# Kernel tuning notes

Hardware: AMD Instinct MI355X
Metric: run time of the kernel (lower is better)

## Reference

```python
import jax, jax.numpy as jnp
import numpy as np

jax.config.update("jax_enable_x64", True)  # torch uses int64 labels with wrapping arithmetic

N = 100_000   # nodes
E = 3_200_000 # edges
D = 128       # label classes (argmax dim)
NUM_ITERATIONS = 3


def setup_inputs() -> dict:
    key = jax.random.key(0)
    k1, k2 = jax.random.split(key)
    x = jax.random.normal(k1, (N, D), dtype=jnp.float32)
    edge_index = jax.random.randint(k2, (2, E), 0, N, dtype=jnp.int64)
    return {"x": x, "edge_index": edge_index}


def _edge_exponents(row):
    """For each edge e, number of edges AFTER e (in edge order) sharing the same row.

    The torch loop computes neighborhood[r] = neighborhood[r]*31 + labels[c]
    sequentially over edges, i.e. for a row-group with targets c_1..c_k (edge order)
    the result is sum_j labels[c_j] * 31**(k - j). The exponent (k - j) is exactly
    the count of later same-row edges.
    """
    e = row.shape[0]
    order = jnp.argsort(row, stable=True)          # stable sort preserves edge order within groups
    srow = row[order]
    first = jnp.searchsorted(srow, srow, side="left")   # group start index
    last = jnp.searchsorted(srow, srow, side="right")   # group end index (exclusive)
    pos = jnp.arange(e) - first                          # position within group
    exp_sorted = (last - first) - 1 - pos                # edges remaining after this one
    return jnp.zeros(e, dtype=jnp.int64).at[order].set(exp_sorted)


def reference(x, edge_index):
    labels = jnp.argmax(x, axis=-1).astype(jnp.int64) if x.ndim > 1 else x.astype(jnp.int64)
    row, col = edge_index[0], edge_index[1]
    exps = _edge_exponents(row)
    # 31**exp in wrapping int64 arithmetic; exponentiation-by-squaring mod 2^64
    # matches the sequential multiply-add mod 2^64 of the torch loop.
    pow31 = jnp.power(jnp.int64(31), exps)
    history = [labels]
    for _ in range(NUM_ITERATIONS):
        vals = labels[col] * pow31                       # [E] per-edge weighted labels
        labels = jax.ops.segment_sum(vals, row, num_segments=N)  # ordered hash accumulate
        history.append(labels)
    return (labels, *history)
```

## Files before the change

kernel.cpp:

```cpp
#include <hip/hip_runtime.h>
#include <hip/hip_bf16.h>


#define WL_D 128
#define NCH 512
#define GRID_F 2048
#define BT 512
#define MSDW 8
#define BBITS 7
#define BROWS 128
#define NBK 1024
#define RLSHIFT 23
#define COLMASK ((1u << RLSHIFT) - 1u)
#define CMAX 5120
#define NBMAX 13
#define KBMAX 10
#define HP8 2487512833u

__device__ inline int xcd_chunk(int bid) { return ((bid & 7) << 6) | (bid >> 3); }

template <int BITS>
__device__ inline unsigned long long match_key(unsigned v) {
    unsigned long long m = ~0ull;
    #pragma unroll
    for (int b = 0; b < BITS; ++b) {
        unsigned long long s = __ballot((v >> b) & 1u);
        m &= ((v >> b) & 1u) ? s : ~s;
    }
    return m;
}

__global__ void __launch_bounds__(BT)
k_hist_argmax(const float* __restrict__ x, const int* __restrict__ ei,
              unsigned* __restrict__ lab0, unsigned* __restrict__ hist,
              int N, int E, int chunk, int nbuckets) {
    __shared__ unsigned h[NBK];
    int bid = blockIdx.x, t = threadIdx.x, lane = t & 63, w = t >> 6;
    if (bid < NCH) {
        int b = xcd_chunk(bid);
        for (int i = t; i < nbuckets; i += BT) h[i] = 0u;
        __syncthreads();
        int base = b * chunk, lim = min(base + chunk, E);
        for (int e = base + t; e < lim; e += BT)
            atomicAdd(&h[((unsigned)ei[e]) >> BBITS], 1u);
        __syncthreads();
        for (int v = t; v < nbuckets; v += BT) hist[(size_t)v * NCH + b] = h[v];
    }
    int half = lane >> 5, li = lane & 31;
    for (int pr = bid * MSDW + w; 2 * pr < N; pr += GRID_F * MSDW) {
        int r = 2 * pr + half;
        float bv = -3.4e38f; int bi = 0;
        if (r < N) {
            float4 v = ((const float4*)(x + (size_t)r * WL_D))[li];
            bv = v.x; bi = 4 * li;
            if (v.y > bv) { bv = v.y; bi = 4 * li + 1; }
            if (v.z > bv) { bv = v.z; bi = 4 * li + 2; }
            if (v.w > bv) { bv = v.w; bi = 4 * li + 3; }
        }
        #pragma unroll
        for (int off = 16; off > 0; off >>= 1) {
            float ov = __shfl_down(bv, off, 32);
            int   oi = __shfl_down(bi, off, 32);
            if (ov > bv || (ov == bv && oi < bi)) { bv = ov; bi = oi; }
        }
        if (li == 0 && r < N) lab0[r] = (unsigned)bi;
    }
}

__global__ void __launch_bounds__(BT)
k_scan_tile(unsigned* __restrict__ hist, unsigned* __restrict__ bsums, int L) {
    __shared__ unsigned smem[BT];
    int b = blockIdx.x, t = threadIdx.x;
    int i0 = b * 1024;
    unsigned v0 = (i0 + 2 * t     < L) ? hist[i0 + 2 * t]     : 0u;
    unsigned v1 = (i0 + 2 * t + 1 < L) ? hist[i0 + 2 * t + 1] : 0u;
    unsigned s = v0 + v1;
    smem[t] = s;
    __syncthreads();
    for (int o = 1; o < BT; o <<= 1) {
        unsigned u = (t >= o) ? smem[t - o] : 0u;
        __syncthreads();
        smem[t] += u;
        __syncthreads();
    }
    unsigned excl = smem[t] - s;
    if (i0 + 2 * t     < L) hist[i0 + 2 * t]     = excl;
    if (i0 + 2 * t + 1 < L) hist[i0 + 2 * t + 1] = excl + v0;
    if (t == BT - 1) bsums[b] = smem[BT - 1];
}

__global__ void __launch_bounds__(BT)
k_transp(const unsigned* __restrict__ hist, const unsigned* __restrict__ bsums,
         unsigned* __restrict__ histT, unsigned* __restrict__ bstart,
         int nbuckets, int ntiles, int E) {
    __shared__ unsigned tl[64][65];
    __shared__ unsigned sb[BT];
    int t = threadIdx.x;
    unsigned my = (t < ntiles) ? bsums[t] : 0u;
    sb[t] = my;
    __syncthreads();
    for (int o = 1; o < BT; o <<= 1) {
        unsigned u = (t >= o) ? sb[t - o] : 0u;
        __syncthreads();
        sb[t] += u;
        __syncthreads();
    }
    sb[t] -= my;
    __syncthreads();
    int vtiles = (nbuckets + 63) / 64;
    int bx = blockIdx.x % vtiles;
    int by = blockIdx.x / vtiles;
    int tx = t & 63, ty = t >> 6;
    int vb = bx * 64, b0 = by * 64;
    #pragma unroll
    for (int r = 0; r < 8; ++r) {
        int row = r * 8 + ty;
        int v = vb + row;
        size_t idx = (size_t)v * NCH + (b0 + tx);
        tl[row][tx] = (v < nbuckets) ? (hist[idx] + sb[idx >> 10]) : 0u;
    }
    __syncthreads();
    #pragma unroll
    for (int r = 0; r < 8; ++r) {
        int row = r * 8 + ty;
        int v = vb + tx;
        if (v < nbuckets) histT[(size_t)(b0 + row) * nbuckets + v] = tl[tx][row];
    }
    if (by == 0 && t < 64) {
        int v = vb + t;
        if (v < nbuckets) bstart[v] = tl[t][0];
    }
    if (blockIdx.x == 0 && t == 64) bstart[nbuckets] = (unsigned)E;
}

__global__ void __launch_bounds__(BT)
k_scatter(const int* __restrict__ ei, const unsigned* __restrict__ histT,
          unsigned* __restrict__ buf, int E, int chunk, int nbuckets) {
    __shared__ unsigned wbase[MSDW * NBK];
    int b = xcd_chunk(blockIdx.x);
    int t = threadIdx.x, lane = t & 63, w = t >> 6;
    unsigned long long lmask = (1ull << lane) - 1ull;
    for (int i = t; i < MSDW * NBK; i += BT) wbase[i] = 0u;
    __syncthreads();
    int base = b * chunk, lim = min(base + chunk, E);
    int sub  = (chunk + MSDW - 1) / MSDW;
    int wbeg = base + w * sub;
    int wend = min(wbeg + sub, lim);
    int nbat = (wbeg < wend) ? ((wend - wbeg + 63) >> 6) : 0;
    unsigned r_[NBMAX];
    #pragma unroll
    for (int k = 0; k < NBMAX; ++k) {
        int e = wbeg + k * 64 + lane;
        r_[k] = (e < wend) ? (unsigned)ei[e] : 0u;
    }
    unsigned long long m_[NBMAX];
    #pragma unroll
    for (int k = 0; k < NBMAX; ++k) {
        if (k >= nbat) break;
        int e = wbeg + k * 64 + lane;
        bool act = (e < wend);
        unsigned v = act ? (r_[k] >> BBITS) : (NBK - 1u);
        unsigned long long m = match_key<10>(v);
        m_[k] = m;
        unsigned before = (unsigned)__popcll(m & lmask);
        if (act && before == 0u) wbase[w * NBK + v] += (unsigned)__popcll(m);
    }
    for (int k = NBMAX; k < nbat; ++k) {
        int e = wbeg + k * 64 + lane;
        bool act = (e < wend);
        unsigned v = act ? (((unsigned)ei[e]) >> BBITS) : (NBK - 1u);
        unsigned long long m = match_key<10>(v);
        unsigned before = (unsigned)__popcll(m & lmask);
        if (act && before == 0u) wbase[w * NBK + v] += (unsigned)__popcll(m);
    }
    __syncthreads();
    for (int v = t; v < nbuckets; v += BT) {
        unsigned g = histT[(size_t)b * nbuckets + v];
        #pragma unroll
        for (int w2 = 0; w2 < MSDW; ++w2) {
            unsigned cnt = wbase[w2 * NBK + v];
            wbase[w2 * NBK + v] = g;
            g += cnt;
        }
    }
    __syncthreads();
    unsigned c_[NBMAX];
    #pragma unroll
    for (int k = 0; k < NBMAX; ++k) {
        int e = wbeg + k * 64 + lane;
        c_[k] = (e < wend) ? (unsigned)ei[(size_t)E + e] : 0u;
    }
    #pragma unroll
    for (int k = 0; k < NBMAX; ++k) {
        if (k >= nbat) break;
        int e = wbeg + k * 64 + lane;
        bool act = (e < wend);
        unsigned r = r_[k], col = c_[k];
        unsigned v = r >> BBITS;
        unsigned long long m = m_[k];
        unsigned before = (unsigned)__popcll(m & lmask);
        int leader = __ffsll(m) - 1;
        unsigned base0 = 0;
        if (act && before == 0u) {
            base0 = wbase[w * NBK + v];
            wbase[w * NBK + v] = base0 + (unsigned)__popcll(m);
        }
        base0 = __shfl(base0, leader, 64);
        if (act) buf[base0 + before] = ((r & (BROWS - 1u)) << RLSHIFT) | col;
    }
    for (int k = NBMAX; k < nbat; ++k) {
        int e = wbeg + k * 64 + lane;
        bool act = (e < wend);
        unsigned r   = act ? (unsigned)ei[e] : 0u;
        unsigned col = act ? (unsigned)ei[(size_t)E + e] : 0u;
        unsigned v = act ? (r >> BBITS) : (NBK - 1u);
        unsigned long long m = match_key<10>(v);
        unsigned before = (unsigned)__popcll(m & lmask);
        unsigned total  = (unsigned)__popcll(m);
        int leader = __ffsll(m) - 1;
        unsigned base0 = 0;
        if (act && before == 0u) { base0 = wbase[w * NBK + v]; wbase[w * NBK + v] = base0 + total; }
        base0 = __shfl(base0, leader, 64);
        if (act) buf[base0 + before] = ((r & (BROWS - 1u)) << RLSHIFT) | col;
    }
}

__global__ void __launch_bounds__(BT)
k_bucket(const unsigned* __restrict__ buf, const unsigned* __restrict__ bstart,
         unsigned* __restrict__ csr, unsigned* __restrict__ rs_g,
         const unsigned* __restrict__ lab0, unsigned* __restrict__ lab1,
         int N, int E, int nbuckets) {
    __shared__ unsigned data2[CMAX];
    __shared__ unsigned h2[MSDW * BROWS];
    __shared__ unsigned offs[BROWS];
    int bb = blockIdx.x, t = threadIdx.x, lane = t & 63, w = t >> 6;
    unsigned long long lmask = (1ull << lane) - 1ull;
    unsigned start = bstart[bb];
    unsigned end   = bstart[bb + 1];
    unsigned len = end - start;
    bool lds_ok = (len <= CMAX);
    for (int i = t; i < MSDW * BROWS; i += BT) h2[i] = 0u;
    __syncthreads();
    unsigned sub  = (len + MSDW - 1u) / MSDW;
    unsigned wbeg = w * sub;
    unsigned wend = min(wbeg + sub, len);
    int nbat = (wbeg < wend) ? (int)((wend - wbeg + 63u) >> 6) : 0;
    unsigned d_[KBMAX];
    #pragma unroll
    for (int k = 0; k < KBMAX; ++k) {
        unsigned i = wbeg + (unsigned)(k * 64 + lane);
        d_[k] = (i < wend) ? buf[start + i] : 0u;
    }
    #pragma unroll
    for (int k = 0; k < KBMAX; ++k) {
        if (k >= nbat) break;
        unsigned i = wbeg + (unsigned)(k * 64 + lane);
        bool act = (i < wend);
        unsigned v = act ? (d_[k] >> RLSHIFT) : 255u;
        unsigned long long m = match_key<8>(v);
        unsigned before = (unsigned)__popcll(m & lmask);
        unsigned total  = (unsigned)__popcll(m);
        if (act && before == 0u) h2[w * BROWS + v] += total;
    }
    for (int k = KBMAX; k < nbat; ++k) {
        unsigned i = wbeg + (unsigned)(k * 64 + lane);
        bool act = (i < wend);
        unsigned v = act ? (buf[start + i] >> RLSHIFT) : 255u;
        unsigned long long m = match_key<8>(v);
        unsigned before = (unsigned)__popcll(m & lmask);
        unsigned total  = (unsigned)__popcll(m);
        if (act && before == 0u) h2[w * BROWS + v] += total;
    }
    __syncthreads();
    unsigned hv = 0;
    if (t < BROWS) {
        #pragma unroll
        for (int w2 = 0; w2 < MSDW; ++w2) hv += h2[w2 * BROWS + t];
        offs[t] = hv;
    }
    __syncthreads();
    for (int o = 1; o < BROWS; o <<= 1) {
        unsigned s = (t < BROWS && t >= o) ? offs[t - o] : 0u;
        __syncthreads();
        if (t < BROWS) offs[t] += s;
        __syncthreads();
    }
    if (t < BROWS) {
        unsigned excl = offs[t] - hv;
        int row = bb * BROWS + t;
        if (row < N) rs_g[row] = start + excl;
        unsigned g = lds_ok ? excl : (start + excl);
        #pragma unroll
        for (int w2 = 0; w2 < MSDW; ++w2) {
            unsigned cnt = h2[w2 * BROWS + t];
            h2[w2 * BROWS + t] = g;
            g += cnt;
        }
    }
    __syncthreads();
    #pragma unroll
    for (int k = 0; k < KBMAX; ++k) {
        if (k >= nbat) break;
        unsigned i = wbeg + (unsigned)(k * 64 + lane);
        bool act = (i < wend);
        unsigned p = d_[k];
        unsigned v = act ? (p >> RLSHIFT) : 255u;
        unsigned long long m = match_key<8>(v);
        unsigned before = (unsigned)__popcll(m & lmask);
        unsigned total  = (unsigned)__popcll(m);
        int leader = __ffsll(m) - 1;
        unsigned base0 = 0;
        if (act && before == 0u) { base0 = h2[w * BROWS + v]; h2[w * BROWS + v] = base0 + total; }
        base0 = __shfl(base0, leader, 64);
        if (act) {
            if (lds_ok) data2[base0 + before] = p & COLMASK;
            else        csr[base0 + before]   = p & COLMASK;
        }
    }
    for (int k = KBMAX; k < nbat; ++k) {
        unsigned i = wbeg + (unsigned)(k * 64 + lane);
        bool act = (i < wend);
        unsigned p = act ? buf[start + i] : 0u;
        unsigned v = act ? (p >> RLSHIFT) : 255u;
        unsigned long long m = match_key<8>(v);
        unsigned before = (unsigned)__popcll(m & lmask);
        unsigned total  = (unsigned)__popcll(m);
        int leader = __ffsll(m) - 1;
        unsigned base0 = 0;
        if (act && before == 0u) { base0 = h2[w * BROWS + v]; h2[w * BROWS + v] = base0 + total; }
        base0 = __shfl(base0, leader, 64);
        if (act) {
            if (lds_ok) data2[base0 + before] = p & COLMASK;
            else        csr[base0 + before]   = p & COLMASK;
        }
    }
    __syncthreads();
    if (lds_ok) for (unsigned i = t; i < len; i += BT) csr[start + i] = data2[i];
    const unsigned H1 = HP8, H2 = HP8 * HP8, H3 = H2 * HP8, H4 = H3 * HP8;
    const unsigned* srcp = lds_ok ? (const unsigned*)data2 : (csr + start);
    int l = t & 7;
    for (int r0 = t >> 3; r0 < BROWS; r0 += BT / 8) {
        unsigned beg = r0 ? offs[r0 - 1] : 0u;
        unsigned d   = offs[r0] - beg;
        unsigned h = 0u;
        unsigned M = (d > (unsigned)l) ? ((d - (unsigned)l + 7u) >> 3) : 0u;
        unsigned bidx = beg + (unsigned)l;
        unsigned m = 0;
        for (; m + 4u <= M; m += 4u) {
            unsigned c0 = srcp[bidx + 8u * m];
            unsigned c1 = srcp[bidx + 8u * m + 8u];
            unsigned c2 = srcp[bidx + 8u * m + 16u];
            unsigned c3 = srcp[bidx + 8u * m + 24u];
            unsigned l0 = lab0[c0], l1 = lab0[c1], l2 = lab0[c2], l3 = lab0[c3];
            h = h * H4 + l0 * H3 + l1 * H2 + l2 * H1 + l3;
        }
        for (; m < M; ++m) h = h * H1 + lab0[srcp[bidx + 8u * m]];
        if (M) {
            unsigned T = d - 1u - (unsigned)l - 8u * (M - 1u);
            unsigned p = ((T & 1u) ? 31u : 1u) * ((T & 2u) ? 961u : 1u)
                       * ((T & 4u) ? 923521u : 1u);
            h *= p;
        }
        h += __shfl_xor(h, 1, 64);
        h += __shfl_xor(h, 2, 64);
        h += __shfl_xor(h, 4, 64);
        int row = bb * BROWS + r0;
        if (l == 0 && row < N) lab1[row] = h;
    }
}

__device__ inline unsigned horner8(const unsigned* __restrict__ csr,
                                   const unsigned* __restrict__ rs,
                                   const unsigned* __restrict__ lin,
                                   int g, int l, int N, int E) {
    const unsigned H1 = HP8, H2 = HP8 * HP8, H3 = H2 * HP8, H4 = H3 * HP8;
    unsigned s = rs[g];
    unsigned e = (g + 1 < N) ? rs[g + 1] : (unsigned)E;
    unsigned d = e - s;
    unsigned h = 0u;
    unsigned M = (d > (unsigned)l) ? ((d - (unsigned)l + 7u) >> 3) : 0u;
    unsigned bidx = s + (unsigned)l;
    unsigned m = 0;
    for (; m + 4u <= M; m += 4u) {
        unsigned c0 = csr[bidx + 8u * m];
        unsigned c1 = csr[bidx + 8u * m + 8u];
        unsigned c2 = csr[bidx + 8u * m + 16u];
        unsigned c3 = csr[bidx + 8u * m + 24u];
        unsigned l0 = lin[c0], l1 = lin[c1], l2 = lin[c2], l3 = lin[c3];
        h = h * H4 + l0 * H3 + l1 * H2 + l2 * H1 + l3;
    }
    for (; m < M; ++m) h = h * H1 + lin[csr[bidx + 8u * m]];
    if (M) {
        unsigned T = d - 1u - (unsigned)l - 8u * (M - 1u);
        unsigned p = ((T & 1u) ? 31u : 1u) * ((T & 2u) ? 961u : 1u)
                   * ((T & 4u) ? 923521u : 1u);
        h *= p;
    }
    h += __shfl_xor(h, 1, 64);
    h += __shfl_xor(h, 2, 64);
    h += __shfl_xor(h, 4, 64);
    return h;
}

__global__ void __launch_bounds__(BT)
k_prop(const unsigned* __restrict__ csr, const unsigned* __restrict__ rs,
       const unsigned* __restrict__ lin, unsigned* __restrict__ lout,
       int N, int E) {
    int idx = blockIdx.x * BT + threadIdx.x;
    int g = idx >> 3, l = idx & 7;
    if (g >= N) return;
    unsigned h = horner8(csr, rs, lin, g, l, N, E);
    if (l == 0) lout[g] = h;
}

__global__ void __launch_bounds__(BT)
k_prop_final(const unsigned* __restrict__ csr, const unsigned* __restrict__ rs,
             const unsigned* __restrict__ lin, const unsigned* __restrict__ l0,
             const unsigned* __restrict__ l1, int* __restrict__ out,
             int N, int E, int pgrid) {
    int idx = blockIdx.x * BT + threadIdx.x;
    int g = idx >> 3, l = idx & 7;
    if (g < N) {
        unsigned h = horner8(csr, rs, lin, g, l, N, E);
        if (l == 0) { out[g] = (int)h; out[4 * N + g] = (int)h; }
    }
    for (int i = idx; i < N; i += pgrid * BT) {
        out[N + i]     = (int)l0[i];
        out[2 * N + i] = (int)l1[i];
        out[3 * N + i] = (int)lin[i];
    }
}

extern "C" void kernel_launch(void* const* d_in, const int* in_sizes, int n_in,
                              void* d_out, int out_size, void* d_ws, size_t ws_size,
                              hipStream_t stream) {
    const float* x  = (const float*)d_in[0];
    const int*   ei = (const int*)d_in[1];
    int* out = (int*)d_out;

    int N = in_sizes[0] / WL_D;
    int E = in_sizes[1] / 2;
    int chunk    = (E + NCH - 1) / NCH;
    int nbuckets = (N + BROWS - 1) / BROWS;
    int L        = nbuckets * NCH;
    int ntiles   = (L + 1023) / 1024;
    int vtiles   = (nbuckets + 63) / 64;
    int btiles   = NCH / 64;
    int pgrid    = (8 * N + BT - 1) / BT;

    unsigned* ws    = (unsigned*)d_ws;
    unsigned* lab0  = ws;
    unsigned* lab1  = lab0 + N;
    unsigned* lab2  = lab1 + N;
    unsigned* rs    = lab2 + N;
    unsigned* bs    = rs + N;
    unsigned* bstart= bs + 1024;
    unsigned* hist  = bstart + 1024;
    unsigned* buf   = hist + L;
    unsigned* csr   = buf + E;
    unsigned* histT = csr;

    k_hist_argmax<<<GRID_F, BT, 0, stream>>>(x, ei, lab0, hist, N, E, chunk, nbuckets);
    k_scan_tile<<<ntiles, BT, 0, stream>>>(hist, bs, L);
    k_transp<<<vtiles * btiles, BT, 0, stream>>>(hist, bs, histT, bstart, nbuckets, ntiles, E);
    k_scatter<<<NCH, BT, 0, stream>>>(ei, histT, buf, E, chunk, nbuckets);
    k_bucket<<<nbuckets, BT, 0, stream>>>(buf, bstart, csr, rs, lab0, lab1, N, E, nbuckets);
    k_prop<<<pgrid, BT, 0, stream>>>(csr, rs, lab1, lab2, N, E);
    k_prop_final<<<pgrid, BT, 0, stream>>>(csr, rs, lab2, lab0, lab1, out, N, E, pgrid);
}
```

Before: 198.6 us.

## Vectorize histogram loads, split argmax blocks, recompute match masks, wave-shuffle scan

```diff
diff --git a/kernel.cpp b/kernel.cpp
--- a/kernel.cpp
+++ b/kernel.cpp
@@ -41,29 +41,42 @@
         for (int i = t; i < nbuckets; i += BT) h[i] = 0u;
         __syncthreads();
         int base = b * chunk, lim = min(base + chunk, E);
-        for (int e = base + t; e < lim; e += BT)
+        int vbeg = (base + 3) & ~3; if (vbeg > lim) vbeg = lim;
+        int vend = lim & ~3;        if (vend < vbeg) vend = vbeg;
+        for (int e = base + t; e < vbeg; e += BT)
             atomicAdd(&h[((unsigned)ei[e]) >> BBITS], 1u);
+        for (int i = vbeg + 4 * t; i < vend; i += 4 * BT) {
+            int4 v4 = *(const int4*)(ei + i);
+            atomicAdd(&h[((unsigned)v4.x) >> BBITS], 1u);
+            atomicAdd(&h[((unsigned)v4.y) >> BBITS], 1u);
+            atomicAdd(&h[((unsigned)v4.z) >> BBITS], 1u);
+            atomicAdd(&h[((unsigned)v4.w) >> BBITS], 1u);
+        }
+        for (int e = vend + t; e < lim; e += BT)
+            atomicAdd(&h[((unsigned)ei[e]) >> BBITS], 1u);
         __syncthreads();
         for (int v = t; v < nbuckets; v += BT) hist[(size_t)v * NCH + b] = h[v];
-    }
-    int half = lane >> 5, li = lane & 31;
-    for (int pr = bid * MSDW + w; 2 * pr < N; pr += GRID_F * MSDW) {
-        int r = 2 * pr + half;
-        float bv = -3.4e38f; int bi = 0;
-        if (r < N) {
-            float4 v = ((const float4*)(x + (size_t)r * WL_D))[li];
-            bv = v.x; bi = 4 * li;
-            if (v.y > bv) { bv = v.y; bi = 4 * li + 1; }
-            if (v.z > bv) { bv = v.z; bi = 4 * li + 2; }
-            if (v.w > bv) { bv = v.w; bi = 4 * li + 3; }
-        }
-        #pragma unroll
-        for (int off = 16; off > 0; off >>= 1) {
-            float ov = __shfl_down(bv, off, 32);
-            int   oi = __shfl_down(bi, off, 32);
-            if (ov > bv || (ov == bv && oi < bi)) { bv = ov; bi = oi; }
-        }
-        if (li == 0 && r < N) lab0[r] = (unsigned)bi;
+    } else {
+        int ab = bid - NCH;
+        int half = lane >> 5, li = lane & 31;
+        for (int pr = ab * MSDW + w; 2 * pr < N; pr += (GRID_F - NCH) * MSDW) {
+            int r = 2 * pr + half;
+            float bv = -3.4e38f; int bi = 0;
+            if (r < N) {
+                float4 v = ((const float4*)(x + (size_t)r * WL_D))[li];
+                bv = v.x; bi = 4 * li;
+                if (v.y > bv) { bv = v.y; bi = 4 * li + 1; }
+                if (v.z > bv) { bv = v.z; bi = 4 * li + 2; }
+                if (v.w > bv) { bv = v.w; bi = 4 * li + 3; }
+            }
+            #pragma unroll
+            for (int off = 16; off > 0; off >>= 1) {
+                float ov = __shfl_down(bv, off, 32);
+                int   oi = __shfl_down(bi, off, 32);
+                if (ov > bv || (ov == bv && oi < bi)) { bv = ov; bi = oi; }
+            }
+            if (li == 0 && r < N) lab0[r] = (unsigned)bi;
+        }
     }
 }
 
@@ -133,7 +146,7 @@
     if (blockIdx.x == 0 && t == 64) bstart[nbuckets] = (unsigned)E;
 }
 
-__global__ void __launch_bounds__(BT)
+__global__ void __launch_bounds__(BT, 6)
 k_scatter(const int* __restrict__ ei, const unsigned* __restrict__ histT,
           unsigned* __restrict__ buf, int E, int chunk, int nbuckets) {
     __shared__ unsigned wbase[MSDW * NBK];
@@ -153,7 +166,6 @@
         int e = wbeg + k * 64 + lane;
         r_[k] = (e < wend) ? (unsigned)ei[e] : 0u;
     }
-    unsigned long long m_[NBMAX];
     #pragma unroll
     for (int k = 0; k < NBMAX; ++k) {
         if (k >= nbat) break;
@@ -161,7 +173,6 @@
         bool act = (e < wend);
         unsigned v = act ? (r_[k] >> BBITS) : (NBK - 1u);
         unsigned long long m = match_key<10>(v);
-        m_[k] = m;
         unsigned before = (unsigned)__popcll(m & lmask);
         if (act && before == 0u) wbase[w * NBK + v] += (unsigned)__popcll(m);
     }
@@ -196,8 +207,8 @@
         int e = wbeg + k * 64 + lane;
         bool act = (e < wend);
         unsigned r = r_[k], col = c_[k];
-        unsigned v = r >> BBITS;
-        unsigned long long m = m_[k];
+        unsigned v = act ? (r >> BBITS) : (NBK - 1u);
+        unsigned long long m = match_key<10>(v);
         unsigned before = (unsigned)__popcll(m & lmask);
         int leader = __ffsll(m) - 1;
         unsigned base0 = 0;
@@ -279,12 +290,19 @@
         offs[t] = hv;
     }
     __syncthreads();
-    for (int o = 1; o < BROWS; o <<= 1) {
-        unsigned s = (t < BROWS && t >= o) ? offs[t - o] : 0u;
-        __syncthreads();
-        if (t < BROWS) offs[t] += s;
-        __syncthreads();
-    }
+    if (t < 64) {
+        unsigned a = offs[t], b2 = offs[t + 64];
+        #pragma unroll
+        for (int o = 1; o < 64; o <<= 1) {
+            unsigned ua = __shfl_up(a, o, 64);
+            unsigned ub = __shfl_up(b2, o, 64);
+            if (t >= o) { a += ua; b2 += ub; }
+        }
+        unsigned tot = __shfl(a, 63, 64);
+        offs[t] = a;
+        offs[t + 64] = b2 + tot;
+    }
+    __syncthreads();
     if (t < BROWS) {
         unsigned excl = offs[t] - hv;
         int row = bb * BROWS + t;
@@ -353,6 +371,11 @@
             unsigned c3 = srcp[bidx + 8u * m + 24u];
             unsigned l0 = lab0[c0], l1 = lab0[c1], l2 = lab0[c2], l3 = lab0[c3];
             h = h * H4 + l0 * H3 + l1 * H2 + l2 * H1 + l3;
+        }
+        for (; m + 2u <= M; m += 2u) {
+            unsigned c0 = srcp[bidx + 8u * m];
+            unsigned c1 = srcp[bidx + 8u * m + 8u];
+            h = h * H2 + lab0[c0] * H1 + lab0[c1];
         }
         for (; m < M; ++m) h = h * H1 + lab0[srcp[bidx + 8u * m]];
         if (M) {
@@ -389,6 +412,11 @@
         unsigned l0 = lin[c0], l1 = lin[c1], l2 = lin[c2], l3 = lin[c3];
         h = h * H4 + l0 * H3 + l1 * H2 + l2 * H1 + l3;
     }
+    for (; m + 2u <= M; m += 2u) {
+        unsigned c0 = csr[bidx + 8u * m];
+        unsigned c1 = csr[bidx + 8u * m + 8u];
+        h = h * H2 + lin[c0] * H1 + lin[c1];
+    }
     for (; m < M; ++m) h = h * H1 + lin[csr[bidx + 8u * m]];
     if (M) {
         unsigned T = d - 1u - (unsigned)l - 8u * (M - 1u);
```

Measured after the change: 197.7 us. No clear change (-0.4%).
